# Performance work log

Hardware: AMD Instinct MI355X
Metric: run time of the kernel (lower is better)

## Reference

```python
import jax, jax.numpy as jnp
import numpy as np

SIZE_SUBMAP = 1024          # points per submap (module global in repo)
RATIO = 0.5                 # CONFIG['Detector']['ratio']
K_POS = int(SIZE_SUBMAP * RATIO)  # 512
K = 32                      # self.k, fps ratio = K / K_POS
B = 2048                    # number of submaps in batch


def fps_single(pts, k):
    """Deterministic farthest point sampling (start at index 0). pts: [n,3] -> [k] int indices."""
    min_d = jnp.sum((pts - pts[0]) ** 2, axis=-1)  # [n]

    def step(min_d, _):
        idx = jnp.argmax(min_d)
        d2 = jnp.sum((pts - pts[idx]) ** 2, axis=-1)
        return jnp.minimum(min_d, d2), idx

    _, idxs = jax.lax.scan(step, min_d, None, length=k - 1)
    return jnp.concatenate([jnp.zeros((1,), dtype=idxs.dtype), idxs])


def setup_inputs() -> dict:
    key = jax.random.key(0)
    ks = jax.random.split(key, 8)
    n = B * SIZE_SUBMAP
    x = jax.random.normal(ks[0], (n, 32), jnp.float32)
    pos = jax.random.normal(ks[1], (n, 3), jnp.float32) * 10.0
    batch = jnp.repeat(jnp.arange(B, dtype=jnp.int32), SIZE_SUBMAP)
    # MLP([32,16,8]) -> Linear(8,1) -> Softplus
    W1 = jax.random.normal(ks[2], (32, 16), jnp.float32) / np.sqrt(32.0)
    b1 = jnp.zeros((16,), jnp.float32)
    W2 = jax.random.normal(ks[3], (16, 8), jnp.float32) / np.sqrt(16.0)
    b2 = jnp.zeros((8,), jnp.float32)
    W3 = jax.random.normal(ks[4], (8, 1), jnp.float32) / np.sqrt(8.0)
    b3 = jnp.zeros((1,), jnp.float32)
    return {"x": x, "pos": pos, "batch": batch,
            "W1": W1, "b1": b1, "W2": W2, "b2": b2, "W3": W3, "b3": b3}


def reference(x, pos, batch, W1, b1, W2, b2, W3, b3):
    bsz = batch.shape[0] // SIZE_SUBMAP  # static batch_size (= batch.max()+1)
    # small per-point MLP + Softplus score
    h = jax.nn.relu(x @ W1 + b1)
    h = jax.nn.relu(h @ W2 + b2)
    s = jax.nn.softplus(h @ W3 + b3)          # [B*N, 1]
    x_batch = s.reshape(bsz, -1)               # [B, N]
    pos_b = pos.reshape(bsz, -1, 3)            # [B, N, 3]
    # distance of xy-coords to submap center
    dist = jnp.linalg.norm(pos_b[..., :2], axis=-1)     # [B, N]
    # k_pos closest points (topk of -dist)
    _, idx1 = jax.lax.top_k(-dist, K_POS)               # [B, K_POS]
    pos_sel = jnp.take_along_axis(pos_b, idx1[..., None], axis=1)  # [B, K_POS, 3]
    # batched farthest point sampling, K points per submap (within-batch indices)
    key_idx = jax.vmap(lambda p: fps_single(p, K))(pos_sel)        # [B, K]
    original_indices = jnp.take_along_axis(idx1, key_idx, axis=1)  # [B, K]
    weights = jnp.take_along_axis(x_batch, original_indices, axis=1)  # [B, K]
    return weights, original_indices
```

## Files before the change

### kernel.cpp

```cpp
#include <hip/hip_runtime.h>
#include <math.h>
#include <stdint.h>

#define N_PTS 1024
#define K_FPS 32

typedef unsigned long long u64;
typedef unsigned int u32;

__device__ __forceinline__ u64 shfl_xor_u64(u64 v, int mask) {
    return __shfl_xor(v, mask, 64);
}

__device__ __forceinline__ int imax2(int a, int b) { return a > b ? a : b; }

template<int CTRL, int RM>
__device__ __forceinline__ int dpp_upd(int v) {
    return __builtin_amdgcn_update_dpp(0, v, CTRL, RM, 0xf, true);
}

template<int M>
__device__ __forceinline__ u64 xshfl(u64 v) {
    if constexpr (M == 32) {
        return shfl_xor_u64(v, 32);
    } else {
        u32 lo = (u32)v, hi = (u32)(v >> 32);
        if constexpr (M == 1) {
            lo = (u32)dpp_upd<0xB1, 0xf>((int)lo);
            hi = (u32)dpp_upd<0xB1, 0xf>((int)hi);
        } else if constexpr (M == 2) {
            lo = (u32)dpp_upd<0x4E, 0xf>((int)lo);
            hi = (u32)dpp_upd<0x4E, 0xf>((int)hi);
        } else {
            constexpr int imm = (M << 10) | 0x1F;
            lo = (u32)__builtin_amdgcn_ds_swizzle((int)lo, imm);
            hi = (u32)__builtin_amdgcn_ds_swizzle((int)hi, imm);
        }
        return ((u64)hi << 32) | lo;
    }
}

template<int J>
__device__ __forceinline__ void intra8(u64 key[8], int L, int k) {
    #pragma unroll
    for (int r = 0; r < 8; ++r) {
        if ((r & J) == 0) {
            const int r2 = r | J;
            int p = (L << 3) | r;
            bool up = ((p & k) == 0);
            u64 a = key[r], c = key[r2];
            bool sw = a < c;
            u64 lo2 = sw ? a : c;
            u64 hi2 = sw ? c : a;
            key[r]  = up ? lo2 : hi2;
            key[r2] = up ? hi2 : lo2;
        }
    }
}

template<int M>
__device__ __forceinline__ void cross8(u64 key[8], int L, int k) {
    bool low = ((L & M) == 0);
    bool up  = ((L & (k >> 3)) == 0);
    bool sel = (low == up);
    #pragma unroll
    for (int r = 0; r < 8; ++r) {
        u64 o = xshfl<M>(key[r]);
        key[r] = ((key[r] < o) == sel) ? key[r] : o;
    }
}

__global__ __launch_bounds__(128) void sortfps_kernel(
    const float* __restrict__ pos,
    float* __restrict__ out_idx,
    int B)
{
#pragma clang fp contract(off)
    const int t    = threadIdx.x;
    const int lane = t & 63;
    const int wv   = t >> 6;
    const int b    = blockIdx.x;

    __shared__ __attribute__((aligned(16))) float spts[N_PTS * 3];
    __shared__ u64 xch[512];

    if (b >= B) return;

    const float* pb = pos + (size_t)b * N_PTS * 3;

    float4 f4[6];
    {
        const float4* pb4 = (const float4*)pb + (size_t)t * 6;
        #pragma unroll
        for (int i = 0; i < 6; ++i) f4[i] = pb4[i];
        float4* sp4 = (float4*)spts + t * 6;
        #pragma unroll
        for (int i = 0; i < 6; ++i) sp4[i] = f4[i];
    }
    const float* f = (const float*)&f4[0];

    u64 key[8];
    #pragma unroll
    for (int r = 0; r < 8; ++r) {
        int p = (t << 3) | r;
        float x = f[r * 3 + 0];
        float y = f[r * 3 + 1];
        float xx = x * x, yy = y * y;
        float d = sqrtf(xx + yy);
        key[r] = ((u64)__float_as_uint(d) << 32) | (u32)p;
    }

    intra8<1>(key, t, 2);
    intra8<2>(key, t, 4);  intra8<1>(key, t, 4);
    intra8<4>(key, t, 8);  intra8<2>(key, t, 8);  intra8<1>(key, t, 8);

    cross8<1>(key, t, 16);
    intra8<4>(key, t, 16); intra8<2>(key, t, 16); intra8<1>(key, t, 16);

    cross8<2>(key, t, 32); cross8<1>(key, t, 32);
    intra8<4>(key, t, 32); intra8<2>(key, t, 32); intra8<1>(key, t, 32);

    cross8<4>(key, t, 64); cross8<2>(key, t, 64); cross8<1>(key, t, 64);
    intra8<4>(key, t, 64); intra8<2>(key, t, 64); intra8<1>(key, t, 64);

    cross8<8>(key, t, 128); cross8<4>(key, t, 128); cross8<2>(key, t, 128);
    cross8<1>(key, t, 128);
    intra8<4>(key, t, 128); intra8<2>(key, t, 128); intra8<1>(key, t, 128);

    cross8<16>(key, t, 256); cross8<8>(key, t, 256); cross8<4>(key, t, 256);
    cross8<2>(key, t, 256);  cross8<1>(key, t, 256);
    intra8<4>(key, t, 256); intra8<2>(key, t, 256); intra8<1>(key, t, 256);

    cross8<32>(key, t, 512); cross8<16>(key, t, 512); cross8<8>(key, t, 512);
    cross8<4>(key, t, 512);  cross8<2>(key, t, 512);  cross8<1>(key, t, 512);
    intra8<4>(key, t, 512); intra8<2>(key, t, 512); intra8<1>(key, t, 512);

    if (wv == 1) {
        #pragma unroll
        for (int r = 0; r < 8; ++r) xch[r * 64 + lane] = key[r];
    }
    __syncthreads();
    if (wv == 1) return;

    #pragma unroll
    for (int r = 0; r < 8; ++r) {
        u64 o = xch[r * 64 + lane];
        key[r] = key[r] < o ? key[r] : o;
    }
    cross8<32>(key, t, 1024); cross8<16>(key, t, 1024); cross8<8>(key, t, 1024);
    cross8<4>(key, t, 1024);  cross8<2>(key, t, 1024);  cross8<1>(key, t, 1024);
    intra8<4>(key, t, 1024); intra8<2>(key, t, 1024); intra8<1>(key, t, 1024);


    float px[8], py[8], pz[8], pidx[8], mind[8];
    #pragma unroll
    for (int r = 0; r < 8; ++r) {
        int o = (int)(u32)key[r];
        const float* sp = &spts[o * 3];
        px[r] = sp[0]; py[r] = sp[1]; pz[r] = sp[2];
        pidx[r] = (float)o;
    }

    float* ob = out_idx + (size_t)b * K_FPS;
    int o0 = __builtin_amdgcn_readfirstlane((int)(u32)key[0]);
    float wx = spts[o0 * 3], wy = spts[o0 * 3 + 1], wz = spts[o0 * 3 + 2];
    float acc = (float)o0;

    #pragma unroll
    for (int r = 0; r < 8; ++r) {
        float dx = px[r] - wx, dy = py[r] - wy, dz = pz[r] - wz;
        float u0 = dx * dx, u1 = dy * dy, u2 = dz * dz;
        mind[r] = (u0 + u1) + u2;
    }

    for (int it = 1; it < K_FPS; ++it) {
        float v4[4], i4[4];
        #pragma unroll
        for (int q = 0; q < 4; ++q) {
            bool g = mind[2 * q + 1] > mind[2 * q];
            v4[q] = g ? mind[2 * q + 1] : mind[2 * q];
            i4[q] = g ? pidx[2 * q + 1] : pidx[2 * q];
        }
        bool s01 = v4[1] > v4[0];
        float va = s01 ? v4[1] : v4[0], ia = s01 ? i4[1] : i4[0];
        bool s23 = v4[3] > v4[2];
        float vb = s23 ? v4[3] : v4[2], ib = s23 ? i4[3] : i4[2];
        bool sab = vb > va;
        float bv = sab ? vb : va, bi = sab ? ib : ia;

        int bvi = __float_as_int(bv);
        int g = bvi;
        g = imax2(g, dpp_upd<0x111, 0xf>(g));
        g = imax2(g, dpp_upd<0x112, 0xf>(g));
        g = imax2(g, dpp_upd<0x114, 0xf>(g));
        g = imax2(g, dpp_upd<0x118, 0xf>(g));
        g = imax2(g, dpp_upd<0x142, 0xa>(g));
        g = imax2(g, dpp_upd<0x143, 0xc>(g));
        int gmax = __builtin_amdgcn_readlane(g, 63);

        u64 mask = __ballot(bvi == gmax);
        int W = __ffsll((unsigned long long)mask) - 1;
        float wi = __uint_as_float(__builtin_amdgcn_readlane(__float_as_uint(bi), W));
        int wo = (int)wi;
        wx = spts[wo * 3]; wy = spts[wo * 3 + 1]; wz = spts[wo * 3 + 2];
        if (lane == it) acc = wi;

        #pragma unroll
        for (int r = 0; r < 8; ++r) {
            float dx = px[r] - wx, dy = py[r] - wy, dz = pz[r] - wz;
            float u0 = dx * dx, u1 = dy * dy, u2 = dz * dz;
            float d2 = (u0 + u1) + u2;
            mind[r] = fminf(mind[r], d2);
        }
    }
    if (lane < K_FPS) ob[lane] = acc;
}

__global__ __launch_bounds__(256) void mlp_kernel(
    const float* __restrict__ x,
    const float* __restrict__ W1, const float* __restrict__ b1,
    const float* __restrict__ W2, const float* __restrict__ b2,
    const float* __restrict__ W3, const float* __restrict__ b3,
    const float* __restrict__ idx_f,
    float* __restrict__ out_w, int total)
{
    __shared__ float sW1[32 * 16];
    __shared__ float sW2[16 * 8];
    __shared__ float sW3[8];
    __shared__ float sb1[16];
    __shared__ float sb2[8];
    __shared__ float sb3;

    for (int i = threadIdx.x; i < 512; i += 256) sW1[i] = W1[i];
    if (threadIdx.x < 128) sW2[threadIdx.x] = W2[threadIdx.x];
    if (threadIdx.x < 16)  sb1[threadIdx.x] = b1[threadIdx.x];
    if (threadIdx.x < 8) {
        sb2[threadIdx.x] = b2[threadIdx.x];
        sW3[threadIdx.x] = W3[threadIdx.x];
    }
    if (threadIdx.x == 0) sb3 = b3[0];
    __syncthreads();

    int t = blockIdx.x * 256 + threadIdx.x;
    if (t >= total) return;

    int b    = t >> 5;
    int orig = (int)(idx_f[t] + 0.5f);
    const float* xr = x + ((size_t)b * N_PTS + (size_t)orig) * 32;

    float xi[32];
    #pragma unroll
    for (int i = 0; i < 32; i += 4) {
        float4 v = *(const float4*)(xr + i);
        xi[i] = v.x; xi[i + 1] = v.y; xi[i + 2] = v.z; xi[i + 3] = v.w;
    }

    float h1[16];
    #pragma unroll
    for (int j = 0; j < 16; ++j) {
        float a = sb1[j];
        #pragma unroll
        for (int i = 0; i < 32; ++i) a += xi[i] * sW1[i * 16 + j];
        h1[j] = fmaxf(a, 0.0f);
    }
    float h2[8];
    #pragma unroll
    for (int j = 0; j < 8; ++j) {
        float a = sb2[j];
        #pragma unroll
        for (int i = 0; i < 16; ++i) a += h1[i] * sW2[i * 8 + j];
        h2[j] = fmaxf(a, 0.0f);
    }
    float v = sb3;
    #pragma unroll
    for (int i = 0; i < 8; ++i) v += h2[i] * sW3[i];

    float sp = fmaxf(v, 0.0f) + log1pf(expf(-fabsf(v)));
    out_w[t] = sp;
}

extern "C" void kernel_launch(void* const* d_in, const int* in_sizes, int n_in,
                              void* d_out, int out_size, void* d_ws, size_t ws_size,
                              hipStream_t stream) {
    const float* x   = (const float*)d_in[0];
    const float* pos = (const float*)d_in[1];
    const float* W1 = (const float*)d_in[3];
    const float* b1 = (const float*)d_in[4];
    const float* W2 = (const float*)d_in[5];
    const float* b2 = (const float*)d_in[6];
    const float* W3 = (const float*)d_in[7];
    const float* b3 = (const float*)d_in[8];

    const int B = in_sizes[2] / N_PTS;
    float* out_w = (float*)d_out;
    float* out_i = (float*)d_out + (size_t)B * K_FPS;

    sortfps_kernel<<<B, 128, 0, stream>>>(pos, out_i, B);

    const int total = B * K_FPS;
    mlp_kernel<<<(total + 255) / 256, 256, 0, stream>>>(
        x, W1, b1, W2, b2, W3, b3, out_i, out_w, total);
}
```

Baseline: 365.2 us.

## Fuse MLP scoring into FPS kernel and broadcast winner coords via readlane

Removes the separate MLP kernel launch and instead evaluates the MLP for the 32 selected points at the end of the sort/FPS kernel, reading weights directly from global memory. The FPS loop now carries the candidate xyz through the argmax reduction and broadcasts them with readlane, which replaces the LDS lookup of the winner's coordinates. In exchange the loop uses more registers, and each block's tail runs the MLP on only 32 lanes with uncached weight loads. Enabling FP contraction in the MLP may change rounding slightly.

Result: no change. 368.0 us (+0.8%).

```diff
diff --git a/kernel.cpp b/kernel.cpp
--- a/kernel.cpp
+++ b/kernel.cpp
@@ -70,8 +70,51 @@
     }
 }
 
+__device__ float mlp_point(const float* __restrict__ xr,
+                           const float* __restrict__ W1, const float* __restrict__ b1,
+                           const float* __restrict__ W2, const float* __restrict__ b2,
+                           const float* __restrict__ W3, const float* __restrict__ b3)
+{
+#pragma clang fp contract(fast)
+    float h1[16];
+    #pragma unroll
+    for (int j = 0; j < 16; ++j) h1[j] = b1[j];
+    #pragma unroll
+    for (int i = 0; i < 32; i += 4) {
+        float4 v = *(const float4*)(xr + i);
+        float xv[4] = {v.x, v.y, v.z, v.w};
+        #pragma unroll
+        for (int q = 0; q < 4; ++q) {
+            #pragma unroll
+            for (int j = 0; j < 16; ++j)
+                h1[j] += xv[q] * W1[(i + q) * 16 + j];
+        }
+    }
+    #pragma unroll
+    for (int j = 0; j < 16; ++j) h1[j] = fmaxf(h1[j], 0.0f);
+
+    float h2[8];
+    #pragma unroll
+    for (int j = 0; j < 8; ++j) {
+        float a = b2[j];
+        #pragma unroll
+        for (int i = 0; i < 16; ++i) a += h1[i] * W2[i * 8 + j];
+        h2[j] = fmaxf(a, 0.0f);
+    }
+    float v = b3[0];
+    #pragma unroll
+    for (int i = 0; i < 8; ++i) v += h2[i] * W3[i];
+
+    return fmaxf(v, 0.0f) + log1pf(expf(-fabsf(v)));
+}
+
 __global__ __launch_bounds__(128) void sortfps_kernel(
     const float* __restrict__ pos,
+    const float* __restrict__ x,
+    const float* __restrict__ W1, const float* __restrict__ b1,
+    const float* __restrict__ W2, const float* __restrict__ b2,
+    const float* __restrict__ W3, const float* __restrict__ b3,
+    float* __restrict__ out_w,
     float* __restrict__ out_idx,
     int B)
 {
@@ -103,9 +146,9 @@
     #pragma unroll
     for (int r = 0; r < 8; ++r) {
         int p = (t << 3) | r;
-        float x = f[r * 3 + 0];
-        float y = f[r * 3 + 1];
-        float xx = x * x, yy = y * y;
+        float xc = f[r * 3 + 0];
+        float yc = f[r * 3 + 1];
+        float xx = xc * xc, yy = yc * yc;
         float d = sqrtf(xx + yy);
         key[r] = ((u64)__float_as_uint(d) << 32) | (u32)p;
     }
@@ -174,19 +217,27 @@
     }
 
     for (int it = 1; it < K_FPS; ++it) {
-        float v4[4], i4[4];
+        float v4[4], i4[4], x4[4], y4[4], z4[4];
         #pragma unroll
         for (int q = 0; q < 4; ++q) {
             bool g = mind[2 * q + 1] > mind[2 * q];
             v4[q] = g ? mind[2 * q + 1] : mind[2 * q];
             i4[q] = g ? pidx[2 * q + 1] : pidx[2 * q];
+            x4[q] = g ? px[2 * q + 1] : px[2 * q];
+            y4[q] = g ? py[2 * q + 1] : py[2 * q];
+            z4[q] = g ? pz[2 * q + 1] : pz[2 * q];
         }
         bool s01 = v4[1] > v4[0];
         float va = s01 ? v4[1] : v4[0], ia = s01 ? i4[1] : i4[0];
+        float xa = s01 ? x4[1] : x4[0], ya = s01 ? y4[1] : y4[0];
+        float za = s01 ? z4[1] : z4[0];
         bool s23 = v4[3] > v4[2];
         float vb = s23 ? v4[3] : v4[2], ib = s23 ? i4[3] : i4[2];
+        float xb = s23 ? x4[3] : x4[2], yb = s23 ? y4[3] : y4[2];
+        float zb = s23 ? z4[3] : z4[2];
         bool sab = vb > va;
         float bv = sab ? vb : va, bi = sab ? ib : ia;
+        float bx = sab ? xb : xa, by = sab ? yb : ya, bz = sab ? zb : za;
 
         int bvi = __float_as_int(bv);
         int g = bvi;
@@ -200,9 +251,10 @@
 
         u64 mask = __ballot(bvi == gmax);
         int W = __ffsll((unsigned long long)mask) - 1;
+        wx = __uint_as_float(__builtin_amdgcn_readlane(__float_as_uint(bx), W));
+        wy = __uint_as_float(__builtin_amdgcn_readlane(__float_as_uint(by), W));
+        wz = __uint_as_float(__builtin_amdgcn_readlane(__float_as_uint(bz), W));
         float wi = __uint_as_float(__builtin_amdgcn_readlane(__float_as_uint(bi), W));
-        int wo = (int)wi;
-        wx = spts[wo * 3]; wy = spts[wo * 3 + 1]; wz = spts[wo * 3 + 2];
         if (lane == it) acc = wi;
 
         #pragma unroll
@@ -213,70 +265,14 @@
             mind[r] = fminf(mind[r], d2);
         }
     }
-    if (lane < K_FPS) ob[lane] = acc;
-}
-
-__global__ __launch_bounds__(256) void mlp_kernel(
-    const float* __restrict__ x,
-    const float* __restrict__ W1, const float* __restrict__ b1,
-    const float* __restrict__ W2, const float* __restrict__ b2,
-    const float* __restrict__ W3, const float* __restrict__ b3,
-    const float* __restrict__ idx_f,
-    float* __restrict__ out_w, int total)
-{
-    __shared__ float sW1[32 * 16];
-    __shared__ float sW2[16 * 8];
-    __shared__ float sW3[8];
-    __shared__ float sb1[16];
-    __shared__ float sb2[8];
-    __shared__ float sb3;
-
-    for (int i = threadIdx.x; i < 512; i += 256) sW1[i] = W1[i];
-    if (threadIdx.x < 128) sW2[threadIdx.x] = W2[threadIdx.x];
-    if (threadIdx.x < 16)  sb1[threadIdx.x] = b1[threadIdx.x];
-    if (threadIdx.x < 8) {
-        sb2[threadIdx.x] = b2[threadIdx.x];
-        sW3[threadIdx.x] = W3[threadIdx.x];
-    }
-    if (threadIdx.x == 0) sb3 = b3[0];
-    __syncthreads();
-
-    int t = blockIdx.x * 256 + threadIdx.x;
-    if (t >= total) return;
-
-    int b    = t >> 5;
-    int orig = (int)(idx_f[t] + 0.5f);
-    const float* xr = x + ((size_t)b * N_PTS + (size_t)orig) * 32;
-
-    float xi[32];
-    #pragma unroll
-    for (int i = 0; i < 32; i += 4) {
-        float4 v = *(const float4*)(xr + i);
-        xi[i] = v.x; xi[i + 1] = v.y; xi[i + 2] = v.z; xi[i + 3] = v.w;
-    }
-
-    float h1[16];
-    #pragma unroll
-    for (int j = 0; j < 16; ++j) {
-        float a = sb1[j];
-        #pragma unroll
-        for (int i = 0; i < 32; ++i) a += xi[i] * sW1[i * 16 + j];
-        h1[j] = fmaxf(a, 0.0f);
-    }
-    float h2[8];
-    #pragma unroll
-    for (int j = 0; j < 8; ++j) {
-        float a = sb2[j];
-        #pragma unroll
-        for (int i = 0; i < 16; ++i) a += h1[i] * sW2[i * 8 + j];
-        h2[j] = fmaxf(a, 0.0f);
-    }
-    float v = sb3;
-    #pragma unroll
-    for (int i = 0; i < 8; ++i) v += h2[i] * sW3[i];
-
-    float sp = fmaxf(v, 0.0f) + log1pf(expf(-fabsf(v)));
-    out_w[t] = sp;
+
+    if (lane < K_FPS) {
+        ob[lane] = acc;
+        int orig = (int)acc;
+        const float* xr = x + ((size_t)b * N_PTS + (size_t)orig) * 32;
+        float w = mlp_point(xr, W1, b1, W2, b2, W3, b3);
+        out_w[(size_t)b * K_FPS + lane] = w;
+    }
 }
 
 extern "C" void kernel_launch(void* const* d_in, const int* in_sizes, int n_in,
@@ -295,9 +291,6 @@
     float* out_w = (float*)d_out;
     float* out_i = (float*)d_out + (size_t)B * K_FPS;
 
-    sortfps_kernel<<<B, 128, 0, stream>>>(pos, out_i, B);
-
-    const int total = B * K_FPS;
-    mlp_kernel<<<(total + 255) / 256, 256, 0, stream>>>(
-        x, W1, b1, W2, b2, W3, b3, out_i, out_w, total);
-}
+    sortfps_kernel<<<B, 128, 0, stream>>>(
+        pos, x, W1, b1, W2, b2, W3, b3, out_w, out_i, B);
+}
```
